# Kernel tuning notes

Hardware: AMD Instinct MI355X
Metric: run time of the kernel (lower is better)

Reference implementation:

```python
import jax, jax.numpy as jnp
import numpy as np

D_MODEL = 2048
N_HEADS = 32
N_KV = 8
HEAD_DIM = D_MODEL // N_HEADS  # 64
D_FF = 8192
ROPE_BASE = 10000.0
EPS = 1e-5
B, S = 2, 2048


def setup_inputs() -> dict:
    key = jax.random.key(0)
    ks = jax.random.split(key, 8)
    s = 0.02
    qkv_out = (N_HEADS + 2 * N_KV) * HEAD_DIM
    return {
        "x": jax.random.normal(ks[0], (B, S, D_MODEL), jnp.float32),
        "w_norm1": jnp.ones((D_MODEL,), jnp.float32),
        "w_qkv": jax.random.normal(ks[1], (D_MODEL, qkv_out), jnp.float32) * s,
        "w_out": jax.random.normal(ks[2], (D_MODEL, D_MODEL), jnp.float32) * s,
        "w_norm2": jnp.ones((D_MODEL,), jnp.float32),
        "w_gate": jax.random.normal(ks[3], (D_MODEL, D_FF), jnp.float32) * s,
        "w_up": jax.random.normal(ks[4], (D_MODEL, D_FF), jnp.float32) * s,
        "w_down": jax.random.normal(ks[5], (D_FF, D_MODEL), jnp.float32) * s,
    }


def _rmsnorm(x, w):
    var = jnp.mean(x * x, axis=-1, keepdims=True)
    return x * jax.lax.rsqrt(var + EPS) * w


def _rope(x, cos, sin):
    # x: [b, s, h, d]; cos/sin: [s, d/2]; non-interleaved (NeoX half split)
    half = x.shape[-1] // 2
    x1, x2 = x[..., :half], x[..., half:]
    c = cos[None, :, None, :]
    sn = sin[None, :, None, :]
    return jnp.concatenate([x1 * c - x2 * sn, x1 * sn + x2 * c], axis=-1)


def _forward(x, w_norm1, w_qkv, w_out, w_norm2, w_gate, w_up, w_down):
    b, s, d = x.shape
    # --- attention block ---
    h = _rmsnorm(x, w_norm1)
    qkv = h @ w_qkv  # [b, s, (H + 2*KV) * hd]
    q = qkv[..., : N_HEADS * HEAD_DIM].reshape(b, s, N_HEADS, HEAD_DIM)
    kv = qkv[..., N_HEADS * HEAD_DIM:].reshape(b, s, 2, N_KV, HEAD_DIM)
    k, v = kv[:, :, 0], kv[:, :, 1]

    inv_freq = 1.0 / (ROPE_BASE ** (jnp.arange(0, HEAD_DIM, 2, dtype=jnp.float32) / HEAD_DIM))
    t = jnp.arange(s, dtype=jnp.float32)
    freqs = t[:, None] * inv_freq[None, :]  # [s, hd/2]
    cos, sin = jnp.cos(freqs), jnp.sin(freqs)
    q = _rope(q, cos, sin)
    k = _rope(k, cos, sin)

    # GQA: repeat_interleave kv heads to match q heads
    g = N_HEADS // N_KV
    k = jnp.repeat(k, g, axis=2)  # [b, s, H, hd]
    v = jnp.repeat(v, g, axis=2)

    scale = 1.0 / np.sqrt(HEAD_DIM)
    scores = jnp.einsum("bqhd,bkhd->bhqk", q, k) * scale
    causal = jnp.tril(jnp.ones((s, s), bool))
    scores = jnp.where(causal[None, None], scores, jnp.finfo(scores.dtype).min)
    attn = jax.nn.softmax(scores, axis=-1)
    ctx = jnp.einsum("bhqk,bkhd->bqhd", attn, v).reshape(b, s, N_HEADS * HEAD_DIM)
    x = x + ctx @ w_out

    # --- MLP block (SwiGLU) ---
    h2 = _rmsnorm(x, w_norm2)
    mlp = (jax.nn.silu(h2 @ w_gate) * (h2 @ w_up)) @ w_down
    return x + mlp


def reference(x, w_norm1, w_qkv, w_out, w_norm2, w_gate, w_up, w_down):
    return _forward(x, w_norm1, w_qkv, w_out, w_norm2, w_gate, w_up, w_down)
```

## Files before the change

kernel.cpp:

```cpp
#include <hip/hip_runtime.h>
#include <stdint.h>

#define D_MODEL 2048
#define S_LEN   2048
#define NTOK    4096
#define QKV_N   3072
#define DFF     8192

typedef float  f32x4   __attribute__((ext_vector_type(4)));
typedef float  f32x16  __attribute__((ext_vector_type(16)));
typedef __bf16 bf16x8  __attribute__((ext_vector_type(8)));
typedef unsigned short u16;
typedef unsigned short u16x8 __attribute__((ext_vector_type(8)));

__device__ __forceinline__ float b2f(u16 u){ union{float f; uint32_t i;} v; v.i = ((uint32_t)u) << 16; return v.f; }
__device__ __forceinline__ u16 f2b(float f){
  union{float f; uint32_t i;} v; v.f = f;
  uint32_t r = v.i + 0x7FFFu + ((v.i >> 16) & 1u);
  return (u16)(r >> 16);
}

__device__ __forceinline__ void gload_lds16(const void* gsrc, void* ldst){
  __builtin_amdgcn_global_load_lds(
      (const __attribute__((address_space(1))) void*)gsrc,
      (__attribute__((address_space(3))) void*)ldst,
      16, 0, 0);
}

__device__ __forceinline__ void conv_tiles(const float* W, u16* WT,
    int Nfull, int Kt, int Nt, int k0g, int n0g, void* ldsbuf)
{
  if (W == nullptr) return;
  float* tf = (float*)ldsbuf;
  const int tt  = threadIdx.x;
  const int nTn = Nt >> 6;
  const int nT  = (Kt >> 6) * nTn;
  const int bid = (blockIdx.z * gridDim.y + blockIdx.y) * gridDim.x + blockIdx.x;
  const int gsz = gridDim.x * gridDim.y * gridDim.z;
  const int c4 = (tt & 15) << 2;
  const int r  = tt >> 4;
  for (int tile = bid; tile < nT; tile += gsz) {
    const int k0 = (tile / nTn) << 6, n0 = (tile % nTn) << 6;
    __syncthreads();
    if (tt < 256) {
#pragma unroll
      for (int i = 0; i < 4; ++i) {
        int row = r + i * 16;
        float4 v = *reinterpret_cast<const float4*>(&W[(size_t)(k0g + k0 + row) * Nfull + n0g + n0 + c4]);
        tf[row * 65 + c4 + 0] = v.x; tf[row * 65 + c4 + 1] = v.y;
        tf[row * 65 + c4 + 2] = v.z; tf[row * 65 + c4 + 3] = v.w;
      }
    }
    __syncthreads();
    if (tt < 256) {
#pragma unroll
      for (int i = 0; i < 4; ++i) {
        int n = r + i * 16;
        ushort4 ov;
        ov.x = f2b(tf[(c4 + 0) * 65 + n]); ov.y = f2b(tf[(c4 + 1) * 65 + n]);
        ov.z = f2b(tf[(c4 + 2) * 65 + n]); ov.w = f2b(tf[(c4 + 3) * 65 + n]);
        *reinterpret_cast<ushort4*>(&WT[(size_t)(n0 + n) * Kt + k0 + c4]) = ov;
      }
    }
  }
}

__global__ __launch_bounds__(256) void wconv_kernel(const float* __restrict__ W, u16* __restrict__ WT,
                                                    int Nfull, int Kt, int Nt, int k0g, int n0g)
{
  __shared__ float tile[64 * 65];
  conv_tiles(W, WT, Nfull, Kt, Nt, k0g, n0g, tile);
}

__global__ void sincos_kernel(float* __restrict__ ct, float* __restrict__ st)
{
  int idx = blockIdx.x * 256 + threadIdx.x;
  if (idx >= S_LEN * 32) return;
  int p = idx >> 5, i = idx & 31;
  double freq = pow(10000.0, -((double)(2*i)) / 64.0);
  double ang  = (double)p * freq;
  ct[idx] = (float)cos(ang);
  st[idx] = (float)sin(ang);
}

template<bool BF16IN>
__global__ __launch_bounds__(256) void rmsnorm_kernel(const void* __restrict__ xin, const float* __restrict__ w, u16* __restrict__ out,
                                                      float* __restrict__ xout,
                                                      const float* cvW, u16* cvWT, int cvNfull, int cvKt, int cvNt, int cvK0g, int cvN0g)
{
  __shared__ float tfbuf[64 * 65];
  const int row = blockIdx.x;
  const int t = threadIdx.x;
  float v[8];
  if (BF16IN) {
    const u16* xr = ((const u16*)xin) + (size_t)row * D_MODEL;
    u16x8 a = *reinterpret_cast<const u16x8*>(&xr[t*8]);
#pragma unroll
    for (int j = 0; j < 8; ++j) v[j] = b2f(a[j]);
  } else {
    const float* xr = ((const float*)xin) + (size_t)row * D_MODEL;
    float4 a = *reinterpret_cast<const float4*>(&xr[t*8]);
    float4 c = *reinterpret_cast<const float4*>(&xr[t*8+4]);
    v[0]=a.x; v[1]=a.y; v[2]=a.z; v[3]=a.w; v[4]=c.x; v[5]=c.y; v[6]=c.z; v[7]=c.w;
  }
  if (xout) {
    float4 o0 = {v[0], v[1], v[2], v[3]};
    float4 o1 = {v[4], v[5], v[6], v[7]};
    *reinterpret_cast<float4*>(&xout[(size_t)row * D_MODEL + t*8])     = o0;
    *reinterpret_cast<float4*>(&xout[(size_t)row * D_MODEL + t*8 + 4]) = o1;
  }
  float ss = 0.f;
#pragma unroll
  for (int j = 0; j < 8; ++j) ss += v[j]*v[j];
#pragma unroll
  for (int d = 1; d < 64; d <<= 1) ss += __shfl_xor(ss, d);
  __shared__ float red[4];
  if ((t & 63) == 0) red[t >> 6] = ss;
  __syncthreads();
  ss = red[0] + red[1] + red[2] + red[3];
  const float sc = rsqrtf(ss * (1.0f / (float)D_MODEL) + 1e-5f);
  float4 w0 = *reinterpret_cast<const float4*>(&w[t*8]);
  float4 w1 = *reinterpret_cast<const float4*>(&w[t*8+4]);
  u16x8 o;
  o[0]=f2b(v[0]*sc*w0.x); o[1]=f2b(v[1]*sc*w0.y); o[2]=f2b(v[2]*sc*w0.z); o[3]=f2b(v[3]*sc*w0.w);
  o[4]=f2b(v[4]*sc*w1.x); o[5]=f2b(v[5]*sc*w1.y); o[6]=f2b(v[6]*sc*w1.z); o[7]=f2b(v[7]*sc*w1.w);
  *reinterpret_cast<u16x8*>(&out[(size_t)row * D_MODEL + t*8]) = o;
  conv_tiles(cvW, cvWT, cvNfull, cvKt, cvNt, cvK0g, cvN0g, tfbuf);
}

template<int EPI>
__device__ __forceinline__ void epi_store(size_t idx, float v, float* Cf, u16* Cb,
                                          const float* resf, const u16* resb, const u16* other)
{
  if (EPI == 2)      Cb[idx] = f2b(v / (1.0f + __expf(-v)));
  else if (EPI == 3) Cb[idx] = f2b(v * b2f(other[idx]));
  else if (EPI == 4) Cb[idx] = f2b(v);
  else if (EPI == 5) Cf[idx] += v;
  else if (EPI == 6) Cb[idx] = f2b(v + resf[idx]);
  else if (EPI == 7) Cf[idx] = v + b2f(resb[idx]);
  else if (EPI == 8) { if (blockIdx.z == 0) Cf[idx] += v; else Cb[idx] = f2b(v); }
}

template<int EPI>
__global__ __launch_bounds__(512, 2) void gemm8p_kernel(
    const u16* __restrict__ A, const u16* __restrict__ BT,
    int K, int lda, int ldb, int ldc, int n_off, int kstep,
    float* Cf, u16* Cb,
    const float* __restrict__ resf, const u16* __restrict__ resb, const u16* other,
    const float* cvW, u16* cvWT, int cvNfull, int cvKt, int cvNt, int cvK0g, int cvN0g)
{
  __shared__ u16 lds[65536];
  const int tid = threadIdx.x;
  const int w = tid >> 6, lane = tid & 63;
  const int g = lane >> 4, lr = lane & 15;
  const int wm = w >> 2, wn = w & 3;
  const int bn = blockIdx.x, bm = blockIdx.y;
  const int koff = blockIdx.z * kstep;
  const int NT = K >> 6;
  const int NI = NT >> 1;

  const int srow = tid >> 3;
  const int sg   = (tid & 7) ^ (srow & 7);
  const u16* Asrc = A  + (size_t)(bm * 256) * lda + koff;
  const u16* Bsrc = BT + (size_t)(bn * 256) * ldb + koff;

  const int agc0 = ((0 + g) ^ (lr & 7)) * 8;
  const int agc1 = ((4 + g) ^ (lr & 7)) * 8;

  f32x4 acc[8][4];
#pragma unroll
  for (int i = 0; i < 8; ++i)
#pragma unroll
    for (int j = 0; j < 4; ++j) acc[i][j] = (f32x4){0.f, 0.f, 0.f, 0.f};
  bf16x8 af[4][2], bf0[2][2], bf1[2][2];

#define STAGE_H(isB, h, b, T) do {                                           \
    int tc = ((T) < NT) ? (T) : (NT - 1);                                    \
    const u16* sb = (isB) ? Bsrc : Asrc;                                     \
    const int  sld = (isB) ? ldb : lda;                                      \
    const u16* s0 = sb + (size_t)((h)*128 + srow) * sld + tc*64 + sg*8;      \
    u16* dst = &lds[(b)*32768 + (isB)*16384 + (h)*8192 + tid*8];             \
    gload_lds16(s0, dst);                                                    \
    gload_lds16(s0 + (size_t)64 * sld, dst + 4096);                          \
  } while (0)

#define LOADA(mih, b) { _Pragma("unroll") for (int q = 0; q < 4; ++q) {      \
    const u16* rp = &lds[(b)*32768 + (wm*128 + (mih)*64 + q*16 + lr) * 64];  \
    af[q][0] = *(const bf16x8*)(rp + agc0);                                  \
    af[q][1] = *(const bf16x8*)(rp + agc1); } }

#define LOADB(dst, nih, b) { _Pragma("unroll") for (int nq = 0; nq < 2; ++nq) { \
    const u16* rp = &lds[(b)*32768 + 16384 + (wn*64 + (nih)*32 + nq*16 + lr) * 64]; \
    dst[nq][0] = *(const bf16x8*)(rp + agc0);                                \
    dst[nq][1] = *(const bf16x8*)(rp + agc1); } }

#define MM(mih, nih, BF) {                                                   \
    __builtin_amdgcn_s_setprio(1);                                           \
    _Pragma("unroll") for (int kk = 0; kk < 2; ++kk)                         \
      _Pragma("unroll") for (int q = 0; q < 4; ++q)                          \
        _Pragma("unroll") for (int nq = 0; nq < 2; ++nq)                     \
          acc[(mih)*4+q][(nih)*2+nq] = __builtin_amdgcn_mfma_f32_16x16x32_bf16( \
              af[q][kk], BF[nq][kk], acc[(mih)*4+q][(nih)*2+nq], 0, 0, 0);   \
    __builtin_amdgcn_s_setprio(0); }

#define SYNC_MID  __builtin_amdgcn_s_barrier();                              \
                  asm volatile("s_waitcnt lgkmcnt(0)" ::: "memory");         \
                  __builtin_amdgcn_sched_barrier(0);
#define PHEND     __builtin_amdgcn_s_barrier();
#define PHEND_VM  asm volatile("s_waitcnt vmcnt(4)" ::: "memory");           \
                  __builtin_amdgcn_s_barrier();

  STAGE_H(0, 0, 0, 0); STAGE_H(0, 1, 0, 0);
  STAGE_H(1, 0, 0, 0); STAGE_H(1, 1, 0, 0);
  STAGE_H(1, 0, 1, 1); STAGE_H(1, 1, 1, 1);
  asm volatile("s_waitcnt vmcnt(4)" ::: "memory");
  __builtin_amdgcn_s_barrier();

  for (int i = 0; i < NI; ++i) {
    const int t0 = 2 * i;
    LOADA(0, 0); LOADB(bf0, 0, 0);
    STAGE_H(0, 0, 1, t0 + 1);
    SYNC_MID; MM(0, 0, bf0); PHEND;
    LOADB(bf1, 1, 0);
    STAGE_H(0, 1, 1, t0 + 1);
    SYNC_MID; MM(0, 1, bf1); PHEND;
    LOADA(1, 0);
    STAGE_H(1, 0, 0, t0 + 2);
    SYNC_MID; MM(1, 1, bf1); PHEND;
    STAGE_H(1, 1, 0, t0 + 2);
    SYNC_MID; MM(1, 0, bf0); PHEND_VM;
    LOADA(0, 1); LOADB(bf0, 0, 1);
    STAGE_H(0, 0, 0, t0 + 2);
    SYNC_MID; MM(0, 0, bf0); PHEND;
    LOADB(bf1, 1, 1);
    STAGE_H(0, 1, 0, t0 + 2);
    SYNC_MID; MM(0, 1, bf1); PHEND;
    LOADA(1, 1);
    STAGE_H(1, 0, 1, t0 + 3);
    SYNC_MID; MM(1, 1, bf1); PHEND;
    STAGE_H(1, 1, 1, t0 + 3);
    SYNC_MID; MM(1, 0, bf0); PHEND_VM;
  }
#undef STAGE_H
#undef LOADA
#undef LOADB
#undef MM

#pragma unroll
  for (int mi = 0; mi < 8; ++mi) {
    const int rowOff = (mi >> 2) * 64 + (mi & 3) * 16;
#pragma unroll
    for (int ni = 0; ni < 4; ++ni) {
      const int colOff = (ni >> 1) * 32 + (ni & 1) * 16;
#pragma unroll
      for (int j = 0; j < 4; ++j) {
        int row = bm*256 + wm*128 + rowOff + g*4 + j;
        int col = n_off + bn*256 + wn*64 + colOff + lr;
        epi_store<EPI>((size_t)row * ldc + col, acc[mi][ni][j], Cf, Cb, resf, resb, other);
      }
    }
  }
  conv_tiles(cvW, cvWT, cvNfull, cvKt, cvNt, cvK0g, cvN0g, lds);
}

template<int EPI>
__global__ __launch_bounds__(512) void gemm128_kernel(
    const u16* __restrict__ A, const u16* __restrict__ BT,
    int K, int lda, int ldb, int ldc, int n_off,
    float* Cf, u16* Cb,
    const float* __restrict__ resf, const u16* __restrict__ resb, const u16* other,
    const float* cvW, u16* cvWT, int cvNfull, int cvKt, int cvNt, int cvK0g, int cvN0g)
{
  __shared__ u16 lds[49152];
  const int tid = threadIdx.x;
  const int w = tid >> 6, lane = tid & 63;
  const int g = lane >> 4, lr = lane & 15;
  const int wm = w >> 2, wn = w & 3;
  const int bn = blockIdx.x, bm = blockIdx.y;
  const int NT = K >> 6;
  const int NI = NT >> 1;

  const int srow = tid >> 3;
  const int sg   = (tid & 7) ^ (srow & 7);
  const u16* Asrc = A  + (size_t)(bm * 128) * lda;
  const u16* Bsrc = BT + (size_t)(bn * 256) * ldb;

  const int agc0 = ((0 + g) ^ (lr & 7)) * 8;
  const int agc1 = ((4 + g) ^ (lr & 7)) * 8;

  f32x4 acc[4][4];
#pragma unroll
  for (int i = 0; i < 4; ++i)
#pragma unroll
    for (int j = 0; j < 4; ++j) acc[i][j] = (f32x4){0.f, 0.f, 0.f, 0.f};
  bf16x8 af[2][2], bf0[2][2], bf1[2][2];

#define STAGE_A(b, T) do {                                                   \
    int tc = ((T) < NT) ? (T) : (NT - 1);                                    \
    const u16* s0 = Asrc + (size_t)srow * lda + tc*64 + sg*8;                \
    u16* dst = &lds[(b)*24576 + tid*8];                                      \
    gload_lds16(s0, dst);                                                    \
    gload_lds16(s0 + (size_t)64 * lda, dst + 4096);                          \
  } while (0)

#define STAGE_BH(h, b, T) do {                                               \
    int tc = ((T) < NT) ? (T) : (NT - 1);                                    \
    const u16* s0 = Bsrc + (size_t)((h)*128 + srow) * ldb + tc*64 + sg*8;    \
    u16* dst = &lds[(b)*24576 + 8192 + (h)*8192 + tid*8];                    \
    gload_lds16(s0, dst);                                                    \
    gload_lds16(s0 + (size_t)64 * ldb, dst + 4096);                         \
  } while (0)

#define LOADA(mih, b) { _Pragma("unroll") for (int q = 0; q < 2; ++q) {      \
    const u16* rp = &lds[(b)*24576 + (wm*64 + (mih)*32 + q*16 + lr) * 64];   \
    af[q][0] = *(const bf16x8*)(rp + agc0);                                  \
    af[q][1] = *(const bf16x8*)(rp + agc1); } }

#define LOADB(dst, nih, b) { _Pragma("unroll") for (int nq = 0; nq < 2; ++nq) { \
    const u16* rp = &lds[(b)*24576 + 8192 + (wn*64 + (nih)*32 + nq*16 + lr) * 64]; \
    dst[nq][0] = *(const bf16x8*)(rp + agc0);                                \
    dst[nq][1] = *(const bf16x8*)(rp + agc1); } }

#define MM(mih, nih, BF) {                                                   \
    __builtin_amdgcn_s_setprio(1);                                           \
    _Pragma("unroll") for (int kk = 0; kk < 2; ++kk)                         \
      _Pragma("unroll") for (int q = 0; q < 2; ++q)                          \
        _Pragma("unroll") for (int nq = 0; nq < 2; ++nq)                     \
          acc[(mih)*2+q][(nih)*2+nq] = __builtin_amdgcn_mfma_f32_16x16x32_bf16( \
              af[q][kk], BF[nq][kk], acc[(mih)*2+q][(nih)*2+nq], 0, 0, 0);   \
    __builtin_amdgcn_s_setprio(0); }

  STAGE_A(0, 0); STAGE_BH(0, 0, 0); STAGE_BH(1, 0, 0);
  STAGE_BH(0, 1, 1); STAGE_BH(1, 1, 1);
  asm volatile("s_waitcnt vmcnt(4)" ::: "memory");
  __builtin_amdgcn_s_barrier();

  for (int i = 0; i < NI; ++i) {
    const int t0 = 2 * i;
    LOADA(0, 0); LOADB(bf0, 0, 0);
    STAGE_A(1, t0 + 1);
    SYNC_MID; MM(0, 0, bf0); PHEND;
    LOADB(bf1, 1, 0);
    STAGE_BH(0, 0, t0 + 2);
    SYNC_MID; MM(0, 1, bf1); PHEND;
    LOADA(1, 0);
    STAGE_BH(1, 0, t0 + 2);
    SYNC_MID; MM(1, 1, bf1); PHEND;
    STAGE_A(0, t0 + 2);
    SYNC_MID; MM(1, 0, bf0);
    asm volatile("s_waitcnt vmcnt(6)" ::: "memory");
    __builtin_amdgcn_s_barrier();
    LOADA(0, 1); LOADB(bf0, 0, 1);
    SYNC_MID; MM(0, 0, bf0); PHEND;
    LOADB(bf1, 1, 1);
    STAGE_BH(0, 1, t0 + 3);
    SYNC_MID; MM(0, 1, bf1); PHEND;
    LOADA(1, 1);
    STAGE_BH(1, 1, t0 + 3);
    SYNC_MID; MM(1, 1, bf1); PHEND;
    SYNC_MID; MM(1, 0, bf0);
    asm volatile("s_waitcnt vmcnt(4)" ::: "memory");
    __builtin_amdgcn_s_barrier();
  }
#undef STAGE_A
#undef STAGE_BH
#undef LOADA
#undef LOADB
#undef MM
#undef SYNC_MID
#undef PHEND
#undef PHEND_VM

#pragma unroll
  for (int mi = 0; mi < 4; ++mi) {
    const int rowOff = (mi >> 1) * 32 + (mi & 1) * 16;
#pragma unroll
    for (int ni = 0; ni < 4; ++ni) {
      const int colOff = (ni >> 1) * 32 + (ni & 1) * 16;
#pragma unroll
      for (int j = 0; j < 4; ++j) {
        int row = bm*128 + wm*64 + rowOff + g*4 + j;
        int col = n_off + bn*256 + wn*64 + colOff + lr;
        epi_store<EPI>((size_t)row * ldc + col, acc[mi][ni][j], Cf, Cb, resf, resb, other);
      }
    }
  }
  conv_tiles(cvW, cvWT, cvNfull, cvKt, cvNt, cvK0g, cvN0g, lds);
}

__global__ __launch_bounds__(256) void rope_kernel(
    const u16* __restrict__ qkv, const float* __restrict__ ct, const float* __restrict__ st,
    u16* __restrict__ Kt, u16* __restrict__ VT)
{
  const int tok = blockIdx.x;
  const int b = tok >> 11, s = tok & (S_LEN - 1);
  const int w = threadIdx.x >> 6, lane = threadIdx.x & 63;
  const size_t base = (size_t)tok * QKV_N;
  for (int slot = w; slot < 16; slot += 4) {
    int col = (slot < 8) ? 2048 + slot * 64 : 2560 + (slot - 8) * 64;
    float v = b2f(qkv[base + col + lane]);
    if (slot < 8) {
      int i = lane & 31;
      float c = ct[s * 32 + i], sn = st[s * 32 + i];
      float p = b2f(qkv[base + col + (lane ^ 32)]);
      v = (lane < 32) ? (v * c - p * sn) : (v * c + p * sn);
    }
    u16 ob = f2b(v);
    if (slot < 8) Kt[((size_t)(b * 8 + slot)     * S_LEN + s) * 64 + lane] = ob;
    else          VT[((size_t)(b * 8 + slot - 8) * 64 + lane) * S_LEN + s] = ob;
  }
}

#define ASCALE 0.1803368801111204f
__global__ __launch_bounds__(256, 2) void attn_kernel(
    const u16* __restrict__ qkv, const u16* __restrict__ Kt,
    const u16* __restrict__ VT, u16* __restrict__ ctx,
    const float* __restrict__ ct, const float* __restrict__ st,
    const float* cvW, u16* cvWT, int cvNfull, int cvKt, int cvNt, int cvK0g, int cvN0g)
{
  __shared__ float tfbuf[64 * 65];
  const int bh  = blockIdx.x;
  const int y   = blockIdx.y;
  const int wid = threadIdx.x >> 6;
  const int lane = threadIdx.x & 63;
  const int b = bh >> 5, h = bh & 31;
  const int kvh = (b << 3) + (h >> 2);
  const int jj = y * 4 + wid;
  const int cq = lane & 31;
  const int hi = lane >> 5;

  const u16* Kp = Kt + (size_t)kvh * S_LEN * 64 + cq * 64 + hi * 8;
  const u16* Vbase = VT + (size_t)kvh * 64 * S_LEN + hi * 8;
  const u16* Vp[4];
#pragma unroll
  for (int v = 0; v < 4; ++v)
    Vp[v] = Vbase + (size_t)((v & 1) * 32 + cq) * S_LEN + (v >> 1) * 16;

  __shared__ float xch[4][32];

#define ATT_LOADK(KF, T) { _Pragma("unroll") for (int q_ = 0; q_ < 4; ++q_) \
    KF[q_] = *(const bf16x8*)(Kp + (T) * 2048 + q_ * 16); }
#define ATT_LOADV(VF, T) { _Pragma("unroll") for (int v_ = 0; v_ < 4; ++v_) \
    VF[v_] = *(const bf16x8*)(Vp[v_] + (T) * 32); }

#define ATT_COMPUTE(KF, VF, T) do {                                          \
    f32x16 sA = {}, sB = {};                                                 \
    sA = __builtin_amdgcn_mfma_f32_32x32x16_bf16(KF[0], qf[0], sA, 0, 0, 0); \
    sB = __builtin_amdgcn_mfma_f32_32x32x16_bf16(KF[1], qf[1], sB, 0, 0, 0); \
    sA = __builtin_amdgcn_mfma_f32_32x32x16_bf16(KF[2], qf[2], sA, 0, 0, 0); \
    sB = __builtin_amdgcn_mfma_f32_32x32x16_bf16(KF[3], qf[3], sB, 0, 0, 0); \
    float p[16];                                                             \
    _Pragma("unroll") for (int r = 0; r < 16; ++r) p[r] = sA[r] + sB[r];     \
    if ((T) == nt - 1) {                                                     \
      _Pragma("unroll") for (int r = 0; r < 16; ++r) {                       \
        int kk = (r & 3) + 8 * (r >> 2) + 4 * hi;                            \
        if (kk > cq) p[r] = -1e30f;                                          \
      }                                                                      \
    }                                                                        \
    float m0_ = fmaxf(fmaxf(p[0], p[1]), p[2]);                              \
    float m1_ = fmaxf(fmaxf(p[3], p[4]), p[5]);                              \
    float m2_ = fmaxf(fmaxf(p[6], p[7]), p[8]);                              \
    float m3_ = fmaxf(fmaxf(p[9], p[10]), p[11]);                            \
    float m4_ = fmaxf(fmaxf(p[12], p[13]), p[14]);                           \
    float tmax = fmaxf(fmaxf(fmaxf(m0_, m1_), m2_), fmaxf(fmaxf(m3_, m4_), p[15])); \
    tmax = fmaxf(tmax, __shfl_xor(tmax, 32));                                \
    if (!__all(tmax <= m + 8.0f)) {                                          \
      float mn = fmaxf(m, tmax);                                             \
      float corr = exp2f(m - mn);                                            \
      m = mn;                                                                \
      l *= corr;                                                             \
      if (hi == 0) xch[wid][cq] = corr;                                      \
      asm volatile("s_waitcnt lgkmcnt(0)" ::: "memory");                     \
      __builtin_amdgcn_sched_barrier(0);                                     \
      float4 c0 = *reinterpret_cast<const float4*>(&xch[wid][4 * hi + 0]);   \
      float4 c1 = *reinterpret_cast<const float4*>(&xch[wid][4 * hi + 8]);   \
      float4 c2 = *reinterpret_cast<const float4*>(&xch[wid][4 * hi + 16]);  \
      float4 c3 = *reinterpret_cast<const float4*>(&xch[wid][4 * hi + 24]);  \
      float ca[16] = {c0.x,c0.y,c0.z,c0.w, c1.x,c1.y,c1.z,c1.w,              \
                      c2.x,c2.y,c2.z,c2.w, c3.x,c3.y,c3.z,c3.w};             \
      _Pragma("unroll") for (int r = 0; r < 16; ++r) { o0[r] *= ca[r]; o1[r] *= ca[r]; } \
    }                                                                        \
    _Pragma("unroll") for (int r = 0; r < 16; ++r) p[r] = exp2f(p[r] - m);   \
    {                                                                        \
      float a0 = p[0]+p[1], a1 = p[2]+p[3], a2 = p[4]+p[5], a3 = p[6]+p[7];  \
      float a4 = p[8]+p[9], a5 = p[10]+p[11], a6 = p[12]+p[13], a7 = p[14]+p[15]; \
      float b0_ = a0+a1, b1_ = a2+a3, b2_ = a4+a5, b3_ = a6+a7;              \
      l += (b0_+b1_) + (b2_+b3_);                                            \
    }                                                                        \
    uint32_t wds[8], pw[8];                                                  \
    _Pragma("unroll") for (int j = 0; j < 8; ++j) {                          \
      uint32_t wv;                                                           \
      asm("v_cvt_pk_bf16_f32 %0, %1, %2" : "=v"(wv) : "v"(p[2*j]), "v"(p[2*j+1])); \
      wds[j] = wv;                                                           \
    }                                                                        \
    _Pragma("unroll") for (int j = 0; j < 8; ++j) pw[j] = __shfl_xor(wds[j], 32); \
    union { uint32_t u[4]; bf16x8 v; } pa0, pa1;                             \
    pa0.u[0] = hi ? pw[2]  : wds[0];                                         \
    pa0.u[1] = hi ? pw[3]  : wds[1];                                         \
    pa0.u[2] = hi ? wds[2] : pw[0];                                          \
    pa0.u[3] = hi ? wds[3] : pw[1];                                          \
    pa1.u[0] = hi ? pw[6]  : wds[4];                                         \
    pa1.u[1] = hi ? pw[7]  : wds[5];                                         \
    pa1.u[2] = hi ? wds[6] : pw[4];                                          \
    pa1.u[3] = hi ? wds[7] : pw[5];                                          \
    o0 = __builtin_amdgcn_mfma_f32_32x32x16_bf16(pa0.v, VF[0], o0, 0, 0, 0); \
    o0 = __builtin_amdgcn_mfma_f32_32x32x16_bf16(pa1.v, VF[2], o0, 0, 0, 0); \
    o1 = __builtin_amdgcn_mfma_f32_32x32x16_bf16(pa0.v, VF[1], o1, 0, 0, 0); \
    o1 = __builtin_amdgcn_mfma_f32_32x32x16_bf16(pa1.v, VF[3], o1, 0, 0, 0); \
  } while (0)

#pragma unroll 1
  for (int task = 0; task < 2; ++task) {
    const int qt = task ? (63 - jj) : jj;
    const int q0 = qt << 5;
    const int nt = qt + 1;

    bf16x8 qf[4];
    {
      const u16* Qr = qkv + (size_t)(b * S_LEN + q0 + cq) * QKV_N + h * 64 + hi * 8;
      u16 qr[4][8];
#pragma unroll
      for (int t = 0; t < 4; ++t)
        *reinterpret_cast<u16x8*>(qr[t]) = *reinterpret_cast<const u16x8*>(Qr + t * 16);
      const float* cb = ct + (size_t)(q0 + cq) * 32 + hi * 8;
      const float* sb = st + (size_t)(q0 + cq) * 32 + hi * 8;
      union { u16 u[8]; bf16x8 v; } qo[4];
#pragma unroll
      for (int t = 0; t < 2; ++t) {
        float4 c0 = *reinterpret_cast<const float4*>(cb + 16 * t);
        float4 c1 = *reinterpret_cast<const float4*>(cb + 16 * t + 4);
        float4 s0 = *reinterpret_cast<const float4*>(sb + 16 * t);
        float4 s1 = *reinterpret_cast<const float4*>(sb + 16 * t + 4);
        float cc[8] = {c0.x,c0.y,c0.z,c0.w, c1.x,c1.y,c1.z,c1.w};
        float ssn[8] = {s0.x,s0.y,s0.z,s0.w, s1.x,s1.y,s1.z,s1.w};
#pragma unroll
        for (int i = 0; i < 8; ++i) {
          float lo = b2f(qr[t][i]), hif = b2f(qr[t + 2][i]);
          qo[t].u[i]     = f2b((lo * cc[i] - hif * ssn[i]) * ASCALE);
          qo[t + 2].u[i] = f2b((hif * cc[i] + lo * ssn[i]) * ASCALE);
        }
      }
#pragma unroll
      for (int t = 0; t < 4; ++t) qf[t] = qo[t].v;
    }

    f32x16 o0 = {}, o1 = {};
    float m = -1e30f, l = 0.f;

    bf16x8 kf0[4], kf1[4], vf0[4], vf1[4];
    ATT_LOADK(kf0, 0); ATT_LOADV(vf0, 0);
    for (int t = 0; t < nt; ) {
      if (t + 1 < nt) { ATT_LOADK(kf1, t + 1); ATT_LOADV(vf1, t + 1); }
      ATT_COMPUTE(kf0, vf0, t);
      ++t; if (t >= nt) break;
      if (t + 1 < nt) { ATT_LOADK(kf0, t + 1); ATT_LOADV(vf0, t + 1); }
      ATT_COMPUTE(kf1, vf1, t);
      ++t;
    }

    l += __shfl_xor(l, 32);
    float linv = 1.0f / l;
    if (hi == 0) xch[wid][cq] = linv;
    asm volatile("s_waitcnt lgkmcnt(0)" ::: "memory");
    __builtin_amdgcn_sched_barrier(0);
    float4 n0 = *reinterpret_cast<const float4*>(&xch[wid][4 * hi + 0]);
    float4 n1 = *reinterpret_cast<const float4*>(&xch[wid][4 * hi + 8]);
    float4 n2 = *reinterpret_cast<const float4*>(&xch[wid][4 * hi + 16]);
    float4 n3 = *reinterpret_cast<const float4*>(&xch[wid][4 * hi + 24]);
    float na[16] = {n0.x,n0.y,n0.z,n0.w, n1.x,n1.y,n1.z,n1.w,
                    n2.x,n2.y,n2.z,n2.w, n3.x,n3.y,n3.z,n3.w};
#pragma unroll
    for (int r = 0; r < 16; ++r) {
      int row = (r & 3) + 8 * (r >> 2) + 4 * hi;
      size_t base = (size_t)(b * S_LEN + q0 + row) * D_MODEL + h * 64;
      ctx[base + cq]      = f2b(o0[r] * na[r]);
      ctx[base + 32 + cq] = f2b(o1[r] * na[r]);
    }
  }
#undef ATT_LOADK
#undef ATT_LOADV
#undef ATT_COMPUTE

  conv_tiles(cvW, cvWT, cvNfull, cvKt, cvNt, cvK0g, cvN0g, tfbuf);
}

__global__ __launch_bounds__(256) void add_partials(float* __restrict__ out,
    const u16* __restrict__ tA, const u16* __restrict__ tB)
{
  size_t i = ((size_t)blockIdx.x * 256 + threadIdx.x) * 8;
  u16x8 a = *reinterpret_cast<const u16x8*>(tA + i);
  u16x8 c = *reinterpret_cast<const u16x8*>(tB + i);
  float4 o0 = *reinterpret_cast<const float4*>(out + i);
  float4 o1 = *reinterpret_cast<const float4*>(out + i + 4);
  o0.x += b2f(a[0]) + b2f(c[0]); o0.y += b2f(a[1]) + b2f(c[1]);
  o0.z += b2f(a[2]) + b2f(c[2]); o0.w += b2f(a[3]) + b2f(c[3]);
  o1.x += b2f(a[4]) + b2f(c[4]); o1.y += b2f(a[5]) + b2f(c[5]);
  o1.z += b2f(a[6]) + b2f(c[6]); o1.w += b2f(a[7]) + b2f(c[7]);
  *reinterpret_cast<float4*>(out + i)     = o0;
  *reinterpret_cast<float4*>(out + i + 4) = o1;
}

#define NOCV nullptr, nullptr, 0, 0, 0, 0, 0
extern "C" void kernel_launch(void* const* d_in, const int* in_sizes, int n_in,
                              void* d_out, int out_size, void* d_ws, size_t ws_size,
                              hipStream_t stream)
{
  const float* x     = (const float*)d_in[0];
  const float* wn1   = (const float*)d_in[1];
  const float* wqkv  = (const float*)d_in[2];
  const float* wout  = (const float*)d_in[3];
  const float* wn2   = (const float*)d_in[4];
  const float* wgate = (const float*)d_in[5];
  const float* wup   = (const float*)d_in[6];
  const float* wdown = (const float*)d_in[7];
  float* out = (float*)d_out;
  char* ws = (char*)d_ws;

  float* cosT  = (float*)(ws + 0);
  float* sinT  = (float*)(ws + 262144);
  u16*   slotA = (u16*)  (ws + 524288);
  u16*   slotB = (u16*)  (ws + 17301504);
  u16*   x1b   = (u16*)  (ws + 34078720);
  char*  S     = ws + 50855936;
  u16*   hB    = (u16*)(S + 0);
  u16*   qkvB  = (u16*)(S + 16777216);
  u16*   kB    = (u16*)(S + 41943040);
  u16*   vtB   = (u16*)(S + 46137344);
  u16*   ctxB  = (u16*)(S + 0);
  u16*   h2B   = (u16*)(S + 0);
  u16*   slab  = (u16*)(S + 16777216);
  u16*   tmpA  = x1b;
  u16*   tmpB  = (u16*)(ws + 101187584);

  sincos_kernel<<<dim3(256), 256, 0, stream>>>(cosT, sinT);
  rmsnorm_kernel<false><<<dim3(NTOK), 256, 0, stream>>>(x, wn1, hB, nullptr, NOCV);
  wconv_kernel<<<dim3(1536), 256, 0, stream>>>(wqkv, slotA, 3072, 2048, 3072, 0, 0);

  gemm128_kernel<4><<<dim3(12, 32), 512, 0, stream>>>(hB, slotA, 2048, 2048, 2048, 3072, 0,
      nullptr, qkvB, nullptr, nullptr, nullptr, wout, slotB, 2048, 2048, 2048, 0, 0);
  rope_kernel<<<dim3(NTOK), 256, 0, stream>>>(qkvB, cosT, sinT, kB, vtB);
  attn_kernel<<<dim3(64, 8), 256, 0, stream>>>(qkvB, kB, vtB, ctxB, cosT, sinT,
      wgate, slotA, 8192, 2048, 4096, 0, 0);

  gemm128_kernel<6><<<dim3(8, 32), 512, 0, stream>>>(ctxB, slotB, 2048, 2048, 2048, 2048, 0,
      nullptr, x1b, x, nullptr, nullptr, NOCV);

  rmsnorm_kernel<true><<<dim3(NTOK), 256, 0, stream>>>(x1b, wn2, h2B, out,
      wup, slotB, 8192, 2048, 4096, 0, 0);

  gemm8p_kernel<2><<<dim3(16, 16), 512, 0, stream>>>(h2B, slotA, 2048, 2048, 2048, 4096, 0, 0,
      nullptr, slab, nullptr, nullptr, nullptr, NOCV);
  gemm8p_kernel<3><<<dim3(16, 16), 512, 0, stream>>>(h2B, slotB, 2048, 2048, 2048, 4096, 0, 0,
      nullptr, slab, nullptr, nullptr, slab, wdown, slotA, 2048, 4096, 2048, 0, 0);
  gemm8p_kernel<8><<<dim3(8, 16, 2), 512, 0, stream>>>(slab, slotA, 2048, 4096, 4096, 2048, 0, 2048,
      out, tmpA, nullptr, nullptr, nullptr, wgate, slotB, 8192, 2048, 4096, 0, 4096);
  gemm8p_kernel<2><<<dim3(16, 16), 512, 0, stream>>>(h2B, slotB, 2048, 2048, 2048, 4096, 0, 0,
      nullptr, slab, nullptr, nullptr, nullptr, wup, slotA, 8192, 2048, 4096, 0, 4096);
  gemm8p_kernel<3><<<dim3(16, 16), 512, 0, stream>>>(h2B, slotA, 2048, 2048, 2048, 4096, 0, 0,
      nullptr, slab, nullptr, nullptr, slab, wdown, slotB, 2048, 4096, 2048, 4096, 0);
  gemm8p_kernel<8><<<dim3(8, 16, 2), 512, 0, stream>>>(slab, slotB, 2048, 4096, 4096, 2048, 0, 2048,
      out, tmpB, nullptr, nullptr, nullptr, NOCV);
  add_partials<<<dim3(4096), 256, 0, stream>>>(out, tmpA, tmpB);
}
```

Baseline: 854.5 us.

## Software-pipeline attention QK MFMA and replace split-K down GEMMs with direct accumulate

The attention inner loop now computes the QK scores for the next tile while the softmax and PV work of the current tile runs, with K loads issued two tiles ahead. The score accumulation uses one MFMA chain instead of two partial chains. The down-projection GEMMs switch from split-K gemm8p passes plus a separate add_partials kernel to gemm128 variants that write or accumulate into the output directly. The first variant adds the x1 residual, which removes the bf16 temporary partials and an extra kernel launch. In exchange it loses split-K parallelism (256 blocks instead of two 128x2 grids), and the single MFMA dependency chain is longer.

```diff
diff --git a/kernel.cpp b/kernel.cpp
--- a/kernel.cpp
+++ b/kernel.cpp
@@ -443,14 +443,17 @@
 #define ATT_LOADV(VF, T) { _Pragma("unroll") for (int v_ = 0; v_ < 4; ++v_) \
     VF[v_] = *(const bf16x8*)(Vp[v_] + (T) * 32); }
 
-#define ATT_COMPUTE(KF, VF, T) do {                                          \
-    f32x16 sA = {}, sB = {};                                                 \
-    sA = __builtin_amdgcn_mfma_f32_32x32x16_bf16(KF[0], qf[0], sA, 0, 0, 0); \
-    sB = __builtin_amdgcn_mfma_f32_32x32x16_bf16(KF[1], qf[1], sB, 0, 0, 0); \
-    sA = __builtin_amdgcn_mfma_f32_32x32x16_bf16(KF[2], qf[2], sA, 0, 0, 0); \
-    sB = __builtin_amdgcn_mfma_f32_32x32x16_bf16(KF[3], qf[3], sB, 0, 0, 0); \
+#define ATT_QK(S, KF) do {                                                   \
+    S = (f32x16){};                                                          \
+    S = __builtin_amdgcn_mfma_f32_32x32x16_bf16(KF[0], qf[0], S, 0, 0, 0);   \
+    S = __builtin_amdgcn_mfma_f32_32x32x16_bf16(KF[1], qf[1], S, 0, 0, 0);   \
+    S = __builtin_amdgcn_mfma_f32_32x32x16_bf16(KF[2], qf[2], S, 0, 0, 0);   \
+    S = __builtin_amdgcn_mfma_f32_32x32x16_bf16(KF[3], qf[3], S, 0, 0, 0);   \
+  } while (0)
+
+#define ATT_FIN(S, VF, T) do {                                               \
     float p[16];                                                             \
-    _Pragma("unroll") for (int r = 0; r < 16; ++r) p[r] = sA[r] + sB[r];     \
+    _Pragma("unroll") for (int r = 0; r < 16; ++r) p[r] = S[r];              \
     if ((T) == nt - 1) {                                                     \
       _Pragma("unroll") for (int r = 0; r < 16; ++r) {                       \
         int kk = (r & 3) + 8 * (r >> 2) + 4 * hi;                            \
@@ -547,14 +550,20 @@
     f32x16 o0 = {}, o1 = {};
     float m = -1e30f, l = 0.f;
 
-    bf16x8 kf0[4], kf1[4], vf0[4], vf1[4];
-    ATT_LOADK(kf0, 0); ATT_LOADV(vf0, 0);
+    bf16x8 kfE[4], kfO[4], vfE[4], vfO[4];
+    f32x16 sE, sO;
+    ATT_LOADK(kfE, 0); ATT_LOADV(vfE, 0);
+    if (nt > 1) ATT_LOADK(kfO, 1);
+    ATT_QK(sE, kfE);
+
     for (int t = 0; t < nt; ) {
-      if (t + 1 < nt) { ATT_LOADK(kf1, t + 1); ATT_LOADV(vf1, t + 1); }
-      ATT_COMPUTE(kf0, vf0, t);
+      if (t + 2 < nt) ATT_LOADK(kfE, t + 2);
+      if (t + 1 < nt) { ATT_LOADV(vfO, t + 1); ATT_QK(sO, kfO); }
+      ATT_FIN(sE, vfE, t);
       ++t; if (t >= nt) break;
-      if (t + 1 < nt) { ATT_LOADK(kf0, t + 1); ATT_LOADV(vf0, t + 1); }
-      ATT_COMPUTE(kf1, vf1, t);
+      if (t + 2 < nt) ATT_LOADK(kfO, t + 2);
+      if (t + 1 < nt) { ATT_LOADV(vfE, t + 1); ATT_QK(sE, kfE); }
+      ATT_FIN(sO, vfO, t);
       ++t;
     }
 
@@ -579,25 +588,10 @@
   }
 #undef ATT_LOADK
 #undef ATT_LOADV
-#undef ATT_COMPUTE
+#undef ATT_QK
+#undef ATT_FIN
 
   conv_tiles(cvW, cvWT, cvNfull, cvKt, cvNt, cvK0g, cvN0g, tfbuf);
-}
-
-__global__ __launch_bounds__(256) void add_partials(float* __restrict__ out,
-    const u16* __restrict__ tA, const u16* __restrict__ tB)
-{
-  size_t i = ((size_t)blockIdx.x * 256 + threadIdx.x) * 8;
-  u16x8 a = *reinterpret_cast<const u16x8*>(tA + i);
-  u16x8 c = *reinterpret_cast<const u16x8*>(tB + i);
-  float4 o0 = *reinterpret_cast<const float4*>(out + i);
-  float4 o1 = *reinterpret_cast<const float4*>(out + i + 4);
-  o0.x += b2f(a[0]) + b2f(c[0]); o0.y += b2f(a[1]) + b2f(c[1]);
-  o0.z += b2f(a[2]) + b2f(c[2]); o0.w += b2f(a[3]) + b2f(c[3]);
-  o1.x += b2f(a[4]) + b2f(c[4]); o1.y += b2f(a[5]) + b2f(c[5]);
-  o1.z += b2f(a[6]) + b2f(c[6]); o1.w += b2f(a[7]) + b2f(c[7]);
-  *reinterpret_cast<float4*>(out + i)     = o0;
-  *reinterpret_cast<float4*>(out + i + 4) = o1;
 }
 
 #define NOCV nullptr, nullptr, 0, 0, 0, 0, 0
@@ -629,8 +623,6 @@
   u16*   ctxB  = (u16*)(S + 0);
   u16*   h2B   = (u16*)(S + 0);
   u16*   slab  = (u16*)(S + 16777216);
-  u16*   tmpA  = x1b;
-  u16*   tmpB  = (u16*)(ws + 101187584);
 
   sincos_kernel<<<dim3(256), 256, 0, stream>>>(cosT, sinT);
   rmsnorm_kernel<false><<<dim3(NTOK), 256, 0, stream>>>(x, wn1, hB, nullptr, NOCV);
@@ -645,20 +637,19 @@
   gemm128_kernel<6><<<dim3(8, 32), 512, 0, stream>>>(ctxB, slotB, 2048, 2048, 2048, 2048, 0,
       nullptr, x1b, x, nullptr, nullptr, NOCV);
 
-  rmsnorm_kernel<true><<<dim3(NTOK), 256, 0, stream>>>(x1b, wn2, h2B, out,
+  rmsnorm_kernel<true><<<dim3(NTOK), 256, 0, stream>>>(x1b, wn2, h2B, nullptr,
       wup, slotB, 8192, 2048, 4096, 0, 0);
 
   gemm8p_kernel<2><<<dim3(16, 16), 512, 0, stream>>>(h2B, slotA, 2048, 2048, 2048, 4096, 0, 0,
       nullptr, slab, nullptr, nullptr, nullptr, NOCV);
   gemm8p_kernel<3><<<dim3(16, 16), 512, 0, stream>>>(h2B, slotB, 2048, 2048, 2048, 4096, 0, 0,
       nullptr, slab, nullptr, nullptr, slab, wdown, slotA, 2048, 4096, 2048, 0, 0);
-  gemm8p_kernel<8><<<dim3(8, 16, 2), 512, 0, stream>>>(slab, slotA, 2048, 4096, 4096, 2048, 0, 2048,
-      out, tmpA, nullptr, nullptr, nullptr, wgate, slotB, 8192, 2048, 4096, 0, 4096);
+  gemm128_kernel<7><<<dim3(8, 32), 512, 0, stream>>>(slab, slotA, 4096, 4096, 4096, 2048, 0,
+      out, nullptr, nullptr, x1b, nullptr, wgate, slotB, 8192, 2048, 4096, 0, 4096);
   gemm8p_kernel<2><<<dim3(16, 16), 512, 0, stream>>>(h2B, slotB, 2048, 2048, 2048, 4096, 0, 0,
       nullptr, slab, nullptr, nullptr, nullptr, wup, slotA, 8192, 2048, 4096, 0, 4096);
   gemm8p_kernel<3><<<dim3(16, 16), 512, 0, stream>>>(h2B, slotA, 2048, 2048, 2048, 4096, 0, 0,
       nullptr, slab, nullptr, nullptr, slab, wdown, slotB, 2048, 4096, 2048, 4096, 0);
-  gemm8p_kernel<8><<<dim3(8, 16, 2), 512, 0, stream>>>(slab, slotB, 2048, 4096, 4096, 2048, 0, 2048,
-      out, tmpB, nullptr, nullptr, nullptr, NOCV);
-  add_partials<<<dim3(4096), 256, 0, stream>>>(out, tmpA, tmpB);
-}
+  gemm128_kernel<5><<<dim3(8, 32), 512, 0, stream>>>(slab, slotB, 4096, 4096, 4096, 2048, 0,
+      out, nullptr, nullptr, nullptr, nullptr, NOCV);
+}
```

After: 792.0 us. 7.3% less time.
